# Kernel tuning notes

Hardware: AMD Instinct MI355X
Metric: run time of the kernel (lower is better)

## Reference

```python
import jax, jax.numpy as jnp
import numpy as np

R = 8
EPS = 1e-08

def _diff_x(c, r):
    # c: (..., H, W), summed along H (axis -2)
    left = c[..., r:2 * r + 1, :]
    middle = c[..., 2 * r + 1:, :] - c[..., :-2 * r - 1, :]
    right = c[..., -1:, :] - c[..., -2 * r - 1:-r - 1, :]
    return jnp.concatenate([left, middle, right], axis=-2)

def _diff_y(c, r):
    left = c[..., :, r:2 * r + 1]
    middle = c[..., :, 2 * r + 1:] - c[..., :, :-2 * r - 1]
    right = c[..., :, -1:] - c[..., :, -2 * r - 1:-r - 1]
    return jnp.concatenate([left, middle, right], axis=-1)

def boxfilter(x, r):
    # summed-area-table box sum over the last two axes
    return _diff_y(_diff_x(jnp.cumsum(x, axis=-2), r).cumsum(axis=-1), r)

def setup_inputs() -> dict:
    key = jax.random.key(0)
    k1, k2 = jax.random.split(key)
    n, t, c, h, w = 4, 8, 3, 512, 512
    inp = jax.random.uniform(k1, (n, t, c, h, w), dtype=jnp.float32)
    ref = jax.random.uniform(k2, (n, t, c, h, w), dtype=jnp.float32)
    return {"input": inp, "ref": ref}

def reference(input, ref):
    n, t, c, h, w = input.shape
    assert h > 2 * R + 1 and w > 2 * R + 1
    # NOTE: faithful to the original: y = input (ref is only shape-checked)
    x = input.reshape(n * t, c, h, w)  # vectorize the per-timestep loop
    N = boxfilter(jnp.ones((1, 1, h, w), dtype=input.dtype), R)  # window counts
    mean_x = boxfilter(x, R) / N
    mean_y = mean_x  # y == x in original code
    cov_xy = boxfilter(x * x, R) / N - mean_x * mean_y
    var_x = boxfilter(x * x, R) / N - mean_x * mean_x
    A = cov_xy / (var_x + EPS)
    b = mean_y - A * mean_x
    mean_A = boxfilter(A, R) / N
    mean_b = boxfilter(b, R) / N
    out = mean_A * x + mean_b
    return out.reshape(n, t, c, h, w)
```

## Files before the change

kernel.cpp:

```cpp
#include <hip/hip_runtime.h>


#define RR   8
#define DD   17
#define WW   512
#define HH   512
#define BHH  32
#define NT   64
#define CPT  8
#define NSLOT 66
#define FEPS 1e-8f

union F4 { float4 v; float f[4]; };

__device__ __forceinline__ float frcp(float a) { return __builtin_amdgcn_rcpf(a); }

#define LFENCE() do { asm volatile("s_waitcnt lgkmcnt(0)" ::: "memory"); \
                      __builtin_amdgcn_sched_barrier(0); } while (0)

__device__ __forceinline__ void hwin(const float4* __restrict__ ev,
                                     const float4* __restrict__ od,
                                     int l, float* w)
{
    F4 a, b, c, d, e, g;
    a.v = ev[l];     b.v = od[l];
    c.v = ev[l + 1]; d.v = od[l + 1];
    e.v = ev[l + 2]; g.v = od[l + 2];
#pragma unroll
    for (int t = 0; t < 4; ++t) {
        w[t]      = a.f[t]; w[4 + t]  = b.f[t];
        w[8 + t]  = c.f[t]; w[12 + t] = d.f[t];
        w[16 + t] = e.f[t]; w[20 + t] = g.f[t];
    }
}

__device__ __forceinline__ void stage1(const float4* ev1, const float4* od1,
                                       const float4* ev2, const float4* od2,
                                       int j, int l, const float* inv_nx,
                                       float* Af, float* Bf)
{
    float w1[24], w2[24];
    hwin(ev1, od1, l, w1);
    hwin(ev2, od2, l, w2);
    float S1[CPT], S2[CPT];
    float s1 = 0.f, s2 = 0.f;
#pragma unroll
    for (int q = 0; q < DD; ++q) { s1 += w1[q]; s2 += w2[q]; }
    S1[0] = s1; S2[0] = s2;
#pragma unroll
    for (int k = 1; k < CPT; ++k) {
        S1[k] = S1[k-1] - w1[k-1] + w1[k-1+DD];
        S2[k] = S2[k-1] - w2[k-1] + w2[k-1+DD];
    }
    const int   ny    = min(HH - 1, j + RR) - max(0, j - RR) + 1;
    const float invny = frcp((float)ny);
#pragma unroll
    for (int k = 0; k < CPT; ++k) {
        float invN = invny * inv_nx[k];
        float mean = S1[k] * invN;
        float ex2  = S2[k] * invN;
        float var  = ex2 - mean * mean;
        float A    = var * frcp(var + FEPS);
        Af[k] = A;
        Bf[k] = mean - A * mean;
    }
}

__global__ __launch_bounds__(NT, 2) void gf_kernel(
    const float* __restrict__ x, float* __restrict__ out)
{
    __shared__ float4 EV[6][NSLOT];
    __shared__ float4 OD[6][NSLOT];

    const int l   = threadIdx.x;
    const int img = blockIdx.y;
    const int r0  = blockIdx.x * BHH;
    const float* px = x   + (size_t)img * (HH * WW);
    float*       po = out + (size_t)img * (HH * WW);
    const int c0 = l * CPT;

    if (l < 24) {
        const int buf = l >> 2, s = l & 3;
        const float4 z = make_float4(0.f, 0.f, 0.f, 0.f);
        if      (s == 0) EV[buf][0]         = z;
        else if (s == 1) OD[buf][0]         = z;
        else if (s == 2) EV[buf][NSLOT - 1] = z;
        else             OD[buf][NSLOT - 1] = z;
    }

    float inv_nx[CPT];
#pragma unroll
    for (int k = 0; k < CPT; ++k) {
        int c  = c0 + k;
        int nx = min(WW - 1, c + RR) - max(0, c - RR) + 1;
        inv_nx[k] = frcp((float)nx);
    }

    float v1[CPT]  = {0,0,0,0,0,0,0,0}, v2[CPT]  = {0,0,0,0,0,0,0,0};
    float v1d[CPT] = {0,0,0,0,0,0,0,0}, v2d[CPT] = {0,0,0,0,0,0,0,0};
    float va[CPT]  = {0,0,0,0,0,0,0,0}, vb[CPT]  = {0,0,0,0,0,0,0,0};

    const int rstart  = max(0, r0 - 2 * RR);
    const int rstart2 = max(0, r0 - RR);
    const int i2max   = r0 + BHH - 1;
    const int i1max   = min(HH - 1, i2max + RR);
    const int rend    = i2max + 2 * RR;

    F4 xr_c[2], xm_c[2], xdd_c[2];
#pragma unroll
    for (int h = 0; h < 2; ++h) {
        xr_c[h].v = make_float4(0,0,0,0);
        xm_c[h].v = make_float4(0,0,0,0);
        xdd_c[h].v = make_float4(0,0,0,0);
    }
    {
        const float* p = px + (size_t)rstart * WW + c0;
        xr_c[0].v = *(const float4*)(p);
        xr_c[1].v = *(const float4*)(p + 4);
    }

#pragma unroll 1
    for (int r = rstart; r <= rend; ++r) {
        const int  i1    = r - RR;
        const int  jd    = i1 - DD;
        const int  i2    = r - 2 * RR;
        const bool addV  = (r < HH);
        const bool subV  = (r - DD   >= rstart);
        const bool subVd = (r - 2*DD >= rstart);
        const bool addA  = (i1 >= rstart2) && (i1 <= i1max);
        const bool subA  = (jd >= rstart2);
        const bool st2   = (i2 >= r0);

        const int rn = r + 1;
        F4 xr_n[2] = {xr_c[0], xr_c[1]};
        F4 xm_n[2] = {xm_c[0], xm_c[1]};
        F4 xdd_n[2] = {xdd_c[0], xdd_c[1]};
        if (rn < HH && rn <= rend) {
            const float* p = px + (size_t)rn * WW + c0;
            xr_n[0].v = *(const float4*)(p); xr_n[1].v = *(const float4*)(p + 4);
        }
        if (rn - DD >= rstart && rn <= rend) {
            const float* p = px + (size_t)(rn - DD) * WW + c0;
            xm_n[0].v = *(const float4*)(p); xm_n[1].v = *(const float4*)(p + 4);
        }
        if (rn - 2*DD >= rstart && rn <= rend) {
            const float* p = px + (size_t)(rn - 2*DD) * WW + c0;
            xdd_n[0].v = *(const float4*)(p); xdd_n[1].v = *(const float4*)(p + 4);
        }
        F4 xi[2];
        if (st2) {
            const float* p = px + (size_t)i2 * WW + c0;
            xi[0].v = *(const float4*)(p); xi[1].v = *(const float4*)(p + 4);
        }

#pragma unroll
        for (int k = 0; k < CPT; ++k) {
            const float xa = xr_c[k >> 2].f[k & 3];
            const float xb = xm_c[k >> 2].f[k & 3];
            const float xc = xdd_c[k >> 2].f[k & 3];
            if (addV)  { v1[k]  += xa; v2[k]  += xa * xa; }
            if (subV)  { v1[k]  -= xb; v2[k]  -= xb * xb; }
            if (subV)  { v1d[k] += xb; v2d[k] += xb * xb; }
            if (subVd) { v1d[k] -= xc; v2d[k] -= xc * xc; }
        }
        {
            F4 t;
#pragma unroll
            for (int e = 0; e < 4; ++e) t.f[e] = v1[e];
            EV[0][1 + l] = t.v;
#pragma unroll
            for (int e = 0; e < 4; ++e) t.f[e] = v1[4 + e];
            OD[0][1 + l] = t.v;
#pragma unroll
            for (int e = 0; e < 4; ++e) t.f[e] = v2[e];
            EV[1][1 + l] = t.v;
#pragma unroll
            for (int e = 0; e < 4; ++e) t.f[e] = v2[4 + e];
            OD[1][1 + l] = t.v;
#pragma unroll
            for (int e = 0; e < 4; ++e) t.f[e] = v1d[e];
            EV[2][1 + l] = t.v;
#pragma unroll
            for (int e = 0; e < 4; ++e) t.f[e] = v1d[4 + e];
            OD[2][1 + l] = t.v;
#pragma unroll
            for (int e = 0; e < 4; ++e) t.f[e] = v2d[e];
            EV[3][1 + l] = t.v;
#pragma unroll
            for (int e = 0; e < 4; ++e) t.f[e] = v2d[4 + e];
            OD[3][1 + l] = t.v;
        }
        LFENCE();

        if (addA) {
            float Af[CPT], Bf[CPT];
            stage1(EV[0], OD[0], EV[1], OD[1], i1, l, inv_nx, Af, Bf);
#pragma unroll
            for (int k = 0; k < CPT; ++k) { va[k] += Af[k]; vb[k] += Bf[k]; }
        }
        if (subA) {
            float Af[CPT], Bf[CPT];
            stage1(EV[2], OD[2], EV[3], OD[3], jd, l, inv_nx, Af, Bf);
#pragma unroll
            for (int k = 0; k < CPT; ++k) { va[k] -= Af[k]; vb[k] -= Bf[k]; }
        }
        if (st2) {
            F4 t;
#pragma unroll
            for (int e = 0; e < 4; ++e) t.f[e] = va[e];
            EV[4][1 + l] = t.v;
#pragma unroll
            for (int e = 0; e < 4; ++e) t.f[e] = va[4 + e];
            OD[4][1 + l] = t.v;
#pragma unroll
            for (int e = 0; e < 4; ++e) t.f[e] = vb[e];
            EV[5][1 + l] = t.v;
#pragma unroll
            for (int e = 0; e < 4; ++e) t.f[e] = vb[4 + e];
            OD[5][1 + l] = t.v;
        }
        LFENCE();

        if (st2) {
            float wa[24], wb[24];
            hwin(EV[4], OD[4], l, wa);
            hwin(EV[5], OD[5], l, wb);
            float SA[CPT], SB[CPT];
            float sa = 0.f, sb = 0.f;
#pragma unroll
            for (int q = 0; q < DD; ++q) { sa += wa[q]; sb += wb[q]; }
            SA[0] = sa; SB[0] = sb;
#pragma unroll
            for (int k = 1; k < CPT; ++k) {
                SA[k] = SA[k-1] - wa[k-1] + wa[k-1+DD];
                SB[k] = SB[k-1] - wb[k-1] + wb[k-1+DD];
            }
            const int   ny2   = min(HH - 1, i2 + RR) - max(0, i2 - RR) + 1;
            const float invny = frcp((float)ny2);
            F4 o0, o1;
#pragma unroll
            for (int k = 0; k < CPT; ++k) {
                float invN = invny * inv_nx[k];
                float ov   = (SA[k] * invN) * xi[k >> 2].f[k & 3] + SB[k] * invN;
                if (k < 4) o0.f[k] = ov; else o1.f[k - 4] = ov;
            }
            float* p = po + (size_t)i2 * WW + c0;
            *(float4*)(p)     = o0.v;
            *(float4*)(p + 4) = o1.v;
        }

        xr_c[0] = xr_n[0];  xr_c[1] = xr_n[1];
        xm_c[0] = xm_n[0];  xm_c[1] = xm_n[1];
        xdd_c[0] = xdd_n[0]; xdd_c[1] = xdd_n[1];
    }
}

extern "C" void kernel_launch(void* const* d_in, const int* in_sizes, int n_in,
                              void* d_out, int out_size, void* d_ws, size_t ws_size,
                              hipStream_t stream) {
    const float* x  = (const float*)d_in[0];
    float* out      = (float*)d_out;
    const int nimg  = in_sizes[0] / (HH * WW);
    dim3 grid(HH / BHH, nimg);
    gf_kernel<<<grid, NT, 0, stream>>>(x, out);
}
```

Baseline: 275.0 us.

## Replace LDS halo exchange with DPP wave shifts for horizontal box windows

The horizontal window gather now gets neighbour lanes' column sums through DPP wave_shr1/wave_shl1 cross-lane moves, with bound_ctrl supplying the zero padding at the edges. This replaces staging them through shared memory. All LDS buffers, their zero-padding setup, the LDS stores and the lgkmcnt fences are removed. Shared-memory latency and waits leave the per-row critical path, at the cost of more VALU DPP moves per row. It relies on the 64-thread block being exactly one wavefront, and on wave-level DPP shifts being supported on the target.

```diff
diff --git a/kernel.cpp b/kernel.cpp
--- a/kernel.cpp
+++ b/kernel.cpp
@@ -8,40 +8,39 @@
 #define BHH  32
 #define NT   64
 #define CPT  8
-#define NSLOT 66
 #define FEPS 1e-8f
 
 union F4 { float4 v; float f[4]; };
 
 __device__ __forceinline__ float frcp(float a) { return __builtin_amdgcn_rcpf(a); }
 
-#define LFENCE() do { asm volatile("s_waitcnt lgkmcnt(0)" ::: "memory"); \
-                      __builtin_amdgcn_sched_barrier(0); } while (0)
-
-__device__ __forceinline__ void hwin(const float4* __restrict__ ev,
-                                     const float4* __restrict__ od,
-                                     int l, float* w)
-{
-    F4 a, b, c, d, e, g;
-    a.v = ev[l];     b.v = od[l];
-    c.v = ev[l + 1]; d.v = od[l + 1];
-    e.v = ev[l + 2]; g.v = od[l + 2];
-#pragma unroll
-    for (int t = 0; t < 4; ++t) {
-        w[t]      = a.f[t]; w[4 + t]  = b.f[t];
-        w[8 + t]  = c.f[t]; w[12 + t] = d.f[t];
-        w[16 + t] = e.f[t]; w[20 + t] = g.f[t];
-    }
-}
-
-__device__ __forceinline__ void stage1(const float4* ev1, const float4* od1,
-                                       const float4* ev2, const float4* od2,
-                                       int j, int l, const float* inv_nx,
+__device__ __forceinline__ float dpp_shr1(float x) {
+    int i = __builtin_bit_cast(int, x);
+    int r = __builtin_amdgcn_update_dpp(0, i, 0x138, 0xF, 0xF, true);
+    return __builtin_bit_cast(float, r);
+}
+__device__ __forceinline__ float dpp_shl1(float x) {
+    int i = __builtin_bit_cast(int, x);
+    int r = __builtin_amdgcn_update_dpp(0, i, 0x130, 0xF, 0xF, true);
+    return __builtin_bit_cast(float, r);
+}
+
+__device__ __forceinline__ void hwin(const float* v, float* w) {
+#pragma unroll
+    for (int k = 0; k < CPT; ++k) {
+        w[k]       = dpp_shr1(v[k]);
+        w[8 + k]   = v[k];
+        w[16 + k]  = dpp_shl1(v[k]);
+    }
+}
+
+__device__ __forceinline__ void stage1(const float* v1, const float* v2,
+                                       int j, const float* inv_nx,
                                        float* Af, float* Bf)
 {
     float w1[24], w2[24];
-    hwin(ev1, od1, l, w1);
-    hwin(ev2, od2, l, w2);
+    hwin(v1, w1);
+    hwin(v2, w2);
     float S1[CPT], S2[CPT];
     float s1 = 0.f, s2 = 0.f;
 #pragma unroll
@@ -69,24 +68,12 @@
 __global__ __launch_bounds__(NT, 2) void gf_kernel(
     const float* __restrict__ x, float* __restrict__ out)
 {
-    __shared__ float4 EV[6][NSLOT];
-    __shared__ float4 OD[6][NSLOT];
-
     const int l   = threadIdx.x;
     const int img = blockIdx.y;
     const int r0  = blockIdx.x * BHH;
     const float* px = x   + (size_t)img * (HH * WW);
     float*       po = out + (size_t)img * (HH * WW);
     const int c0 = l * CPT;
-
-    if (l < 24) {
-        const int buf = l >> 2, s = l & 3;
-        const float4 z = make_float4(0.f, 0.f, 0.f, 0.f);
-        if      (s == 0) EV[buf][0]         = z;
-        else if (s == 1) OD[buf][0]         = z;
-        else if (s == 2) EV[buf][NSLOT - 1] = z;
-        else             OD[buf][NSLOT - 1] = z;
-    }
 
     float inv_nx[CPT];
 #pragma unroll
@@ -163,68 +150,24 @@
             if (subV)  { v1d[k] += xb; v2d[k] += xb * xb; }
             if (subVd) { v1d[k] -= xc; v2d[k] -= xc * xc; }
         }
-        {
-            F4 t;
-#pragma unroll
-            for (int e = 0; e < 4; ++e) t.f[e] = v1[e];
-            EV[0][1 + l] = t.v;
-#pragma unroll
-            for (int e = 0; e < 4; ++e) t.f[e] = v1[4 + e];
-            OD[0][1 + l] = t.v;
-#pragma unroll
-            for (int e = 0; e < 4; ++e) t.f[e] = v2[e];
-            EV[1][1 + l] = t.v;
-#pragma unroll
-            for (int e = 0; e < 4; ++e) t.f[e] = v2[4 + e];
-            OD[1][1 + l] = t.v;
-#pragma unroll
-            for (int e = 0; e < 4; ++e) t.f[e] = v1d[e];
-            EV[2][1 + l] = t.v;
-#pragma unroll
-            for (int e = 0; e < 4; ++e) t.f[e] = v1d[4 + e];
-            OD[2][1 + l] = t.v;
-#pragma unroll
-            for (int e = 0; e < 4; ++e) t.f[e] = v2d[e];
-            EV[3][1 + l] = t.v;
-#pragma unroll
-            for (int e = 0; e < 4; ++e) t.f[e] = v2d[4 + e];
-            OD[3][1 + l] = t.v;
-        }
-        LFENCE();
 
         if (addA) {
             float Af[CPT], Bf[CPT];
-            stage1(EV[0], OD[0], EV[1], OD[1], i1, l, inv_nx, Af, Bf);
+            stage1(v1, v2, i1, inv_nx, Af, Bf);
 #pragma unroll
             for (int k = 0; k < CPT; ++k) { va[k] += Af[k]; vb[k] += Bf[k]; }
         }
         if (subA) {
             float Af[CPT], Bf[CPT];
-            stage1(EV[2], OD[2], EV[3], OD[3], jd, l, inv_nx, Af, Bf);
+            stage1(v1d, v2d, jd, inv_nx, Af, Bf);
 #pragma unroll
             for (int k = 0; k < CPT; ++k) { va[k] -= Af[k]; vb[k] -= Bf[k]; }
         }
-        if (st2) {
-            F4 t;
-#pragma unroll
-            for (int e = 0; e < 4; ++e) t.f[e] = va[e];
-            EV[4][1 + l] = t.v;
-#pragma unroll
-            for (int e = 0; e < 4; ++e) t.f[e] = va[4 + e];
-            OD[4][1 + l] = t.v;
-#pragma unroll
-            for (int e = 0; e < 4; ++e) t.f[e] = vb[e];
-            EV[5][1 + l] = t.v;
-#pragma unroll
-            for (int e = 0; e < 4; ++e) t.f[e] = vb[4 + e];
-            OD[5][1 + l] = t.v;
-        }
-        LFENCE();
 
         if (st2) {
             float wa[24], wb[24];
-            hwin(EV[4], OD[4], l, wa);
-            hwin(EV[5], OD[5], l, wb);
+            hwin(va, wa);
+            hwin(vb, wb);
             float SA[CPT], SB[CPT];
             float sa = 0.f, sb = 0.f;
 #pragma unroll
```

After: 277.3 us. No clear change (+0.8%).
